# Optimization experiments

Measured on AMD Instinct MI355X. Metric: run time of the kernel, lower is better.

## Reference

```python
import jax, jax.numpy as jnp
import numpy as np

N, C, H, W = 1024, 16, 32, 32
E = 4096


def setup_inputs() -> dict:
    key = jax.random.key(0)
    ks = jax.random.split(key, 10)
    feats = jax.random.normal(ks[0], (N, C, H, W), dtype=jnp.float32)
    src = jax.random.randint(ks[1], (E,), 0, N)
    dst = jax.random.randint(ks[2], (E,), 0, N)
    sign = jax.random.randint(ks[3], (E,), 0, 2) * 2 - 1  # values in {-1, +1}
    edges = jnp.stack([src, sign, dst], axis=1).astype(jnp.int64)
    s = 0.05
    w1 = jax.random.normal(ks[4], (2 * C, 3 * C, 3, 3), dtype=jnp.float32) * s
    b1 = jnp.zeros((2 * C,), dtype=jnp.float32)
    w2 = jax.random.normal(ks[5], (2 * C, 2 * C, 3, 3), dtype=jnp.float32) * s
    b2 = jnp.zeros((2 * C,), dtype=jnp.float32)
    w3 = jax.random.normal(ks[6], (C, 2 * C, 3, 3), dtype=jnp.float32) * s
    b3 = jnp.zeros((C,), dtype=jnp.float32)
    return {"feats": feats, "edges": edges, "w1": w1, "b1": b1,
            "w2": w2, "b2": b2, "w3": w3, "b3": b3}


def _pool_edges(edges, feats, positive):
    # Bidirectional gather + scatter_add over selected edges.
    # Mask-by-zero keeps shapes static (equivalent math to torch.where selection).
    sign = edges[:, 1]
    mask = (sign > 0) if positive else (sign < 0)
    w = mask.astype(feats.dtype)[:, None, None, None]
    src = edges[:, 0]
    dst = edges[:, 2]
    pooled = jnp.zeros_like(feats)
    pooled = pooled.at[dst].add(feats[src] * w)  # src -> dst
    pooled = pooled.at[src].add(feats[dst] * w)  # dst -> src
    return pooled


def _conv(x, w, b):
    y = jax.lax.conv_general_dilated(
        x, w, window_strides=(1, 1), padding=((1, 1), (1, 1)),
        dimension_numbers=("NCHW", "OIHW", "NCHW"))
    return y + b[None, :, None, None]


def _leaky(x):
    return jax.nn.leaky_relu(x, negative_slope=0.1)


def reference(feats, edges, w1, b1, w2, b2, w3, b3):
    pos = _pool_edges(edges, feats, positive=True)
    neg = _pool_edges(edges, feats, positive=False)
    x = jnp.concatenate([feats, pos, neg], axis=1)  # [N, 3C, H, W]
    x = _leaky(_conv(x, w1, b1))
    x = _leaky(_conv(x, w2, b2))
    x = _leaky(_conv(x, w3, b3))
    return x
```

## Files before the change

kernel.cpp:

```cpp
#include <hip/hip_runtime.h>


#define NIMG 1024
#define CHW  16384
#define NEDGE 4096
#define MAXD 64

#define ICP1 56
#define KP1  456
#define ICP2 40
#define KP2  296
#define XSZ (34*34*ICP1)
#define WSZ (32*KP1)

#define WG1N (32*KP1)
#define WG2N (32*KP2)
#define WG3N (16*KP2)
#define WGTOT (WG1N+WG2N+WG3N)

typedef __attribute__((ext_vector_type(8))) _Float16 half8;
typedef __attribute__((ext_vector_type(4))) _Float16 half4;
typedef __attribute__((ext_vector_type(4))) float float4v;

__device__ __forceinline__ float leaky(float x) { return x > 0.f ? x : 0.1f * x; }

__global__ __launch_bounds__(256) void build_adj(
    const int* __restrict__ edges, int* __restrict__ deg, int* __restrict__ adj,
    const float* __restrict__ w1, const float* __restrict__ w2,
    const float* __restrict__ w3, _Float16* __restrict__ wg)
{
    const int e = blockIdx.x * 256 + threadIdx.x;
    const bool is64 = (edges[1] == 0);
    int s, sg, d;
    if (is64) { s = edges[6*e]; sg = edges[6*e + 2]; d = edges[6*e + 4]; }
    else      { s = edges[3*e]; sg = edges[3*e + 1]; d = edges[3*e + 2]; }
    const int tag_d = (d << 1) | (int)(sg > 0);
    const int tag_s = (s << 1) | (int)(sg > 0);
    int i = atomicAdd(&deg[s], 1); if (i < MAXD) adj[(s << 6) + i] = tag_d;
    int j = atomicAdd(&deg[d], 1); if (j < MAXD) adj[(d << 6) + j] = tag_s;

    for (int t = e; t < WGTOT; t += NEDGE) {
        _Float16 val = (_Float16)0.f;
        if (t < WG1N) {
            int oc = t / KP1, r = t - oc * KP1;
            if (r < 432) { int tap = r / 48, ic = r - tap * 48;
                           val = (_Float16)w1[(oc*48 + ic)*9 + tap]; }
        } else if (t < WG1N + WG2N) {
            int u = t - WG1N;
            int oc = u / KP2, r = u - oc * KP2;
            if (r < 288) { int tap = r / 32, ic = r - tap * 32;
                           val = (_Float16)w2[(oc*32 + ic)*9 + tap]; }
        } else {
            int u = t - (WG1N + WG2N);
            int oc = u / KP2, r = u - oc * KP2;
            if (r < 288) { int tap = r / 32, ic = r - tap * 32;
                           val = (_Float16)w3[(oc*32 + ic)*9 + tap]; }
        }
        wg[t] = val;
    }
}

__global__ __launch_bounds__(256) void transpose_kernel(
    const float* __restrict__ feats, _Float16* __restrict__ fcl)
{
    const int n = blockIdx.x, tid = threadIdx.x;
    const float* fb = feats + (size_t)n * CHW;
    _Float16*    ob = fcl   + (size_t)n * 1024 * 16;
    const int p0 = tid * 4;
    float4v t[16];
    #pragma unroll
    for (int c = 0; c < 16; ++c) t[c] = *(const float4v*)(fb + (c << 10) + p0);
    #pragma unroll
    for (int u = 0; u < 4; ++u) {
        half8 v0, v1;
        #pragma unroll
        for (int c = 0; c < 8; ++c) { v0[c] = (_Float16)t[c][u]; v1[c] = (_Float16)t[c+8][u]; }
        *(half8*)(ob + (p0+u)*16)     = v0;
        *(half8*)(ob + (p0+u)*16 + 8) = v1;
    }
}

__global__ __launch_bounds__(1024, 4) void conv_kernel(
    const _Float16* __restrict__ fcl,
    const int* __restrict__ deg, const int* __restrict__ adj,
    const _Float16* __restrict__ wg,
    const float* __restrict__ b1, const float* __restrict__ b2,
    const float* __restrict__ b3, float* __restrict__ out)
{
    __shared__ __align__(16) _Float16 Xs[XSZ];
    __shared__ __align__(16) _Float16 Ws[WSZ];
    const int n    = blockIdx.x;
    const int tid  = threadIdx.x;
    const int wave = tid >> 6;
    const int lane = tid & 63;
    const int col  = lane & 15;
    const int quad = lane >> 4;

    {
        const half8* fc = (const half8*)(fcl + (size_t)n * CHW);
        const int p = tid;
        const int base = (((p >> 5) + 1)*34 + (p & 31) + 1) * ICP1;
        *(half8*)(Xs + base)     = fc[2*p];
        *(half8*)(Xs + base + 8) = fc[2*p + 1];

        int m = deg[n]; if (m > MAXD) m = MAXD;
        const int* al = adj + (n << 6);
        float ap[16], an[16];
        #pragma unroll
        for (int c = 0; c < 16; ++c) { ap[c] = 0.f; an[c] = 0.f; }
        int i = 0;
        for (; i + 4 <= m; i += 4) {
            int v0 = al[i], v1 = al[i+1], v2 = al[i+2], v3 = al[i+3];
            const half8* f0 = (const half8*)(fcl + (size_t)(v0 >> 1) * CHW);
            const half8* f1 = (const half8*)(fcl + (size_t)(v1 >> 1) * CHW);
            const half8* f2 = (const half8*)(fcl + (size_t)(v2 >> 1) * CHW);
            const half8* f3 = (const half8*)(fcl + (size_t)(v3 >> 1) * CHW);
            half8 x00 = f0[2*p], x01 = f0[2*p+1];
            half8 x10 = f1[2*p], x11 = f1[2*p+1];
            half8 x20 = f2[2*p], x21 = f2[2*p+1];
            half8 x30 = f3[2*p], x31 = f3[2*p+1];
            if (v0 & 1) { for (int c = 0; c < 8; ++c) { ap[c] += (float)x00[c]; ap[c+8] += (float)x01[c]; } }
            else        { for (int c = 0; c < 8; ++c) { an[c] += (float)x00[c]; an[c+8] += (float)x01[c]; } }
            if (v1 & 1) { for (int c = 0; c < 8; ++c) { ap[c] += (float)x10[c]; ap[c+8] += (float)x11[c]; } }
            else        { for (int c = 0; c < 8; ++c) { an[c] += (float)x10[c]; an[c+8] += (float)x11[c]; } }
            if (v2 & 1) { for (int c = 0; c < 8; ++c) { ap[c] += (float)x20[c]; ap[c+8] += (float)x21[c]; } }
            else        { for (int c = 0; c < 8; ++c) { an[c] += (float)x20[c]; an[c+8] += (float)x21[c]; } }
            if (v3 & 1) { for (int c = 0; c < 8; ++c) { ap[c] += (float)x30[c]; ap[c+8] += (float)x31[c]; } }
            else        { for (int c = 0; c < 8; ++c) { an[c] += (float)x30[c]; an[c+8] += (float)x31[c]; } }
        }
        for (; i < m; ++i) {
            const int v = al[i];
            const half8* fb = (const half8*)(fcl + (size_t)(v >> 1) * CHW);
            half8 x0 = fb[2*p], x1 = fb[2*p + 1];
            if (v & 1) {
                #pragma unroll
                for (int c = 0; c < 8; ++c) { ap[c] += (float)x0[c]; ap[c+8] += (float)x1[c]; }
            } else {
                #pragma unroll
                for (int c = 0; c < 8; ++c) { an[c] += (float)x0[c]; an[c+8] += (float)x1[c]; }
            }
        }
        half8 h0, h1, h2, h3;
        #pragma unroll
        for (int c = 0; c < 8; ++c) { h0[c] = (_Float16)ap[c]; h1[c] = (_Float16)ap[c+8];
                                      h2[c] = (_Float16)an[c]; h3[c] = (_Float16)an[c+8]; }
        *(half8*)(Xs + base + 16) = h0;
        *(half8*)(Xs + base + 24) = h1;
        *(half8*)(Xs + base + 32) = h2;
        *(half8*)(Xs + base + 40) = h3;

        {
            const half8* src = (const half8*)wg;
            half8* dst = (half8*)Ws;
            for (int t = tid; t < WG1N/8; t += 1024) dst[t] = src[t];
        }
        if (tid < 132) {
            int hp, wp;
            if      (tid < 34)  { hp = 0;        wp = tid; }
            else if (tid < 68)  { hp = 33;       wp = tid - 34; }
            else if (tid < 100) { hp = tid - 67; wp = 0; }
            else                { hp = tid - 99; wp = 33; }
            int hb = (hp*34 + wp) * ICP1;
            #pragma unroll
            for (int t = 0; t < 6; ++t) *(half8*)(Xs + hb + t*8) = (half8)0;
        }
    }
    __syncthreads();

    float4v acc[2][4];

    {
        #pragma unroll
        for (int m = 0; m < 2; ++m)
            #pragma unroll
            for (int j = 0; j < 4; ++j) acc[m][j] = (float4v){0.f,0.f,0.f,0.f};
        int pixb[4];
        #pragma unroll
        for (int j = 0; j < 4; ++j) {
            int p = wave*64 + j*16 + col;
            pixb[j] = ((p >> 5)*34 + (p & 31)) * ICP1;
        }
        const int abase = col * KP1 + quad * 8;
        #pragma unroll
        for (int ks = 0; ks < 14; ++ks) {
            int kq  = ks*32 + quad*8;
            int tap = kq / 48;
            int off = 0;
            if (tap < 9) {
                int ic0 = kq - tap*48;
                int dh = tap / 3, dw = tap - dh*3;
                off = (dh*34 + dw)*ICP1 + ic0;
            }
            half8 a0 = *(const half8*)(Ws + abase + ks*32);
            half8 a1 = *(const half8*)(Ws + 16*KP1 + abase + ks*32);
            #pragma unroll
            for (int j = 0; j < 4; ++j) {
                half8 b = *(const half8*)(Xs + pixb[j] + off);
                acc[0][j] = __builtin_amdgcn_mfma_f32_16x16x32_f16(a0, b, acc[0][j], 0, 0, 0);
                acc[1][j] = __builtin_amdgcn_mfma_f32_16x16x32_f16(a1, b, acc[1][j], 0, 0, 0);
            }
        }
    }
    __syncthreads();

    {
        if (tid < 132) {
            int hp, wp;
            if      (tid < 34)  { hp = 0;        wp = tid; }
            else if (tid < 68)  { hp = 33;       wp = tid - 34; }
            else if (tid < 100) { hp = tid - 67; wp = 0; }
            else                { hp = tid - 99; wp = 33; }
            int hb = (hp*34 + wp) * ICP2;
            #pragma unroll
            for (int t = 0; t < 4; ++t) *(half8*)(Xs + hb + t*8) = (half8)0;
        }
        float bv[2][4];
        #pragma unroll
        for (int m = 0; m < 2; ++m)
            #pragma unroll
            for (int r = 0; r < 4; ++r) bv[m][r] = b1[m*16 + quad*4 + r];
        #pragma unroll
        for (int m = 0; m < 2; ++m)
            #pragma unroll
            for (int j = 0; j < 4; ++j) {
                int p = wave*64 + j*16 + col;
                _Float16* y = Xs + ((((p>>5)+1)*34) + (p&31) + 1)*ICP2 + m*16 + quad*4;
                half4 v;
                #pragma unroll
                for (int r = 0; r < 4; ++r) v[r] = (_Float16)leaky(acc[m][j][r] + bv[m][r]);
                *(half4*)y = v;
            }
        {
            const half8* src = (const half8*)(wg + WG1N);
            half8* dst = (half8*)Ws;
            for (int t = tid; t < WG2N/8; t += 1024) dst[t] = src[t];
        }
    }
    __syncthreads();

    {
        #pragma unroll
        for (int m = 0; m < 2; ++m)
            #pragma unroll
            for (int j = 0; j < 4; ++j) acc[m][j] = (float4v){0.f,0.f,0.f,0.f};
        int pixb[4];
        #pragma unroll
        for (int j = 0; j < 4; ++j) {
            int p = wave*64 + j*16 + col;
            pixb[j] = ((p >> 5)*34 + (p & 31)) * ICP2;
        }
        const int abase = col * KP2 + quad * 8;
        #pragma unroll
        for (int ks = 0; ks < 9; ++ks) {
            int kq  = ks*32 + quad*8;
            int tap = kq >> 5, ic0 = kq & 31;
            int dh = tap / 3, dw = tap - dh*3;
            int off = (dh*34 + dw)*ICP2 + ic0;
            half8 a0 = *(const half8*)(Ws + abase + ks*32);
            half8 a1 = *(const half8*)(Ws + 16*KP2 + abase + ks*32);
            #pragma unroll
            for (int j = 0; j < 4; ++j) {
                half8 b = *(const half8*)(Xs + pixb[j] + off);
                acc[0][j] = __builtin_amdgcn_mfma_f32_16x16x32_f16(a0, b, acc[0][j], 0, 0, 0);
                acc[1][j] = __builtin_amdgcn_mfma_f32_16x16x32_f16(a1, b, acc[1][j], 0, 0, 0);
            }
        }
    }
    __syncthreads();

    {
        float bv[2][4];
        #pragma unroll
        for (int m = 0; m < 2; ++m)
            #pragma unroll
            for (int r = 0; r < 4; ++r) bv[m][r] = b2[m*16 + quad*4 + r];
        #pragma unroll
        for (int m = 0; m < 2; ++m)
            #pragma unroll
            for (int j = 0; j < 4; ++j) {
                int p = wave*64 + j*16 + col;
                _Float16* y = Xs + ((((p>>5)+1)*34) + (p&31) + 1)*ICP2 + m*16 + quad*4;
                half4 v;
                #pragma unroll
                for (int r = 0; r < 4; ++r) v[r] = (_Float16)leaky(acc[m][j][r] + bv[m][r]);
                *(half4*)y = v;
            }
        {
            const half8* src = (const half8*)(wg + WG1N + WG2N);
            half8* dst = (half8*)Ws;
            for (int t = tid; t < WG3N/8; t += 1024) dst[t] = src[t];
        }
    }
    __syncthreads();

    {
        float4v a3[4];
        #pragma unroll
        for (int j = 0; j < 4; ++j) a3[j] = (float4v){0.f,0.f,0.f,0.f};
        int pixb[4];
        #pragma unroll
        for (int j = 0; j < 4; ++j) {
            int p = wave*64 + j*16 + col;
            pixb[j] = ((p >> 5)*34 + (p & 31)) * ICP2;
        }
        const int abase = col * KP2 + quad * 8;
        #pragma unroll
        for (int ks = 0; ks < 9; ++ks) {
            int kq  = ks*32 + quad*8;
            int tap = kq >> 5, ic0 = kq & 31;
            int dh = tap / 3, dw = tap - dh*3;
            int off = (dh*34 + dw)*ICP2 + ic0;
            half8 a0 = *(const half8*)(Ws + abase + ks*32);
            #pragma unroll
            for (int j = 0; j < 4; ++j) {
                half8 b = *(const half8*)(Xs + pixb[j] + off);
                a3[j] = __builtin_amdgcn_mfma_f32_16x16x32_f16(a0, b, a3[j], 0, 0, 0);
            }
        }
        float bv[4];
        #pragma unroll
        for (int r = 0; r < 4; ++r) bv[r] = b3[quad*4 + r];
        float* op = out + (size_t)n * CHW;
        #pragma unroll
        for (int j = 0; j < 4; ++j) {
            int p = wave*64 + j*16 + col;
            #pragma unroll
            for (int r = 0; r < 4; ++r)
                op[(quad*4 + r)*1024 + p] = leaky(a3[j][r] + bv[r]);
        }
    }
}

extern "C" void kernel_launch(void* const* d_in, const int* in_sizes, int n_in,
                              void* d_out, int out_size, void* d_ws, size_t ws_size,
                              hipStream_t stream) {
    const float* feats = (const float*)d_in[0];
    const int*   edges = (const int*)  d_in[1];
    const float* w1 = (const float*)d_in[2];
    const float* b1 = (const float*)d_in[3];
    const float* w2 = (const float*)d_in[4];
    const float* b2 = (const float*)d_in[5];
    const float* w3 = (const float*)d_in[6];
    const float* b3 = (const float*)d_in[7];
    float* out = (float*)d_out;

    _Float16* fcl = (_Float16*)d_ws;
    int* deg = (int*)((char*)d_ws + (32u << 20));
    int* adj = deg + NIMG;
    _Float16* wg = (_Float16*)((char*)d_ws + (32u << 20) + 4096 + NIMG*MAXD*4);

    hipMemsetAsync(deg, 0, NIMG * sizeof(int), stream);
    build_adj<<<dim3(NEDGE/256), dim3(256), 0, stream>>>(edges, deg, adj, w1, w2, w3, wg);
    transpose_kernel<<<dim3(NIMG), dim3(256), 0, stream>>>(feats, fcl);
    conv_kernel<<<dim3(NIMG), dim3(1024), 0, stream>>>(fcl, deg, adj, wg,
                                                       b1, b2, b3, out);
}
```

Before: 233.3 us.

## Halve conv block size, double pixels per wave, retile weights, merge prep kernels

The transpose and adjacency/weight-packing kernels are merged into one launch, removing a kernel launch. The conv kernel now uses 512 threads, with each wave covering 128 pixels (8 MFMA column tiles) so each A-fragment load is reused across twice as many MFMAs. Weights are repacked into a per-k-step [ks][oc][32] layout to replace the padded row-major layout. Each thread now gathers neighbor sums for two pixels, and register pressure roughly doubles for accumulators, which may reduce occupancy.

```diff
diff --git a/kernel.cpp b/kernel.cpp
--- a/kernel.cpp
+++ b/kernel.cpp
@@ -7,15 +7,13 @@
 #define MAXD 64
 
 #define ICP1 56
-#define KP1  456
 #define ICP2 40
-#define KP2  296
 #define XSZ (34*34*ICP1)
-#define WSZ (32*KP1)
-
-#define WG1N (32*KP1)
-#define WG2N (32*KP2)
-#define WG3N (16*KP2)
+#define WSZ (14*32*32)
+
+#define WG1N (14*32*32)
+#define WG2N (9*32*32)
+#define WG3N (9*16*32)
 #define WGTOT (WG1N+WG2N+WG3N)
 
 typedef __attribute__((ext_vector_type(8))) _Float16 half8;
@@ -24,12 +22,32 @@
 
 __device__ __forceinline__ float leaky(float x) { return x > 0.f ? x : 0.1f * x; }
 
-__global__ __launch_bounds__(256) void build_adj(
+__global__ __launch_bounds__(256) void prep_kernel(
+    const float* __restrict__ feats, _Float16* __restrict__ fcl,
     const int* __restrict__ edges, int* __restrict__ deg, int* __restrict__ adj,
     const float* __restrict__ w1, const float* __restrict__ w2,
     const float* __restrict__ w3, _Float16* __restrict__ wg)
 {
-    const int e = blockIdx.x * 256 + threadIdx.x;
+    const int b = blockIdx.x, tid = threadIdx.x;
+    if (b < NIMG) {
+        const int n = b;
+        const float* fb = feats + (size_t)n * CHW;
+        _Float16*    ob = fcl   + (size_t)n * 1024 * 16;
+        const int p0 = tid * 4;
+        float4v t[16];
+        #pragma unroll
+        for (int c = 0; c < 16; ++c) t[c] = *(const float4v*)(fb + (c << 10) + p0);
+        #pragma unroll
+        for (int u = 0; u < 4; ++u) {
+            half8 v0, v1;
+            #pragma unroll
+            for (int c = 0; c < 8; ++c) { v0[c] = (_Float16)t[c][u]; v1[c] = (_Float16)t[c+8][u]; }
+            *(half8*)(ob + (p0+u)*16)     = v0;
+            *(half8*)(ob + (p0+u)*16 + 8) = v1;
+        }
+        return;
+    }
+    const int e = (b - NIMG) * 256 + tid;
     const bool is64 = (edges[1] == 0);
     int s, sg, d;
     if (is64) { s = edges[6*e]; sg = edges[6*e + 2]; d = edges[6*e + 4]; }
@@ -42,45 +60,28 @@
     for (int t = e; t < WGTOT; t += NEDGE) {
         _Float16 val = (_Float16)0.f;
         if (t < WG1N) {
-            int oc = t / KP1, r = t - oc * KP1;
-            if (r < 432) { int tap = r / 48, ic = r - tap * 48;
+            int ks = t >> 10, oc = (t >> 5) & 31, j32 = t & 31;
+            int k = ks*32 + j32;
+            if (k < 432) { int tap = k / 48, ic = k - tap*48;
                            val = (_Float16)w1[(oc*48 + ic)*9 + tap]; }
         } else if (t < WG1N + WG2N) {
             int u = t - WG1N;
-            int oc = u / KP2, r = u - oc * KP2;
-            if (r < 288) { int tap = r / 32, ic = r - tap * 32;
-                           val = (_Float16)w2[(oc*32 + ic)*9 + tap]; }
+            int ks = u >> 10, oc = (u >> 5) & 31, j32 = u & 31;
+            int k = ks*32 + j32;
+            int tap = k >> 5, ic = k & 31;
+            val = (_Float16)w2[(oc*32 + ic)*9 + tap];
         } else {
             int u = t - (WG1N + WG2N);
-            int oc = u / KP2, r = u - oc * KP2;
-            if (r < 288) { int tap = r / 32, ic = r - tap * 32;
-                           val = (_Float16)w3[(oc*32 + ic)*9 + tap]; }
+            int ks = u >> 9, oc = (u >> 5) & 15, j32 = u & 31;
+            int k = ks*32 + j32;
+            int tap = k >> 5, ic = k & 31;
+            val = (_Float16)w3[(oc*32 + ic)*9 + tap];
         }
         wg[t] = val;
     }
 }
 
-__global__ __launch_bounds__(256) void transpose_kernel(
-    const float* __restrict__ feats, _Float16* __restrict__ fcl)
-{
-    const int n = blockIdx.x, tid = threadIdx.x;
-    const float* fb = feats + (size_t)n * CHW;
-    _Float16*    ob = fcl   + (size_t)n * 1024 * 16;
-    const int p0 = tid * 4;
-    float4v t[16];
-    #pragma unroll
-    for (int c = 0; c < 16; ++c) t[c] = *(const float4v*)(fb + (c << 10) + p0);
-    #pragma unroll
-    for (int u = 0; u < 4; ++u) {
-        half8 v0, v1;
-        #pragma unroll
-        for (int c = 0; c < 8; ++c) { v0[c] = (_Float16)t[c][u]; v1[c] = (_Float16)t[c+8][u]; }
-        *(half8*)(ob + (p0+u)*16)     = v0;
-        *(half8*)(ob + (p0+u)*16 + 8) = v1;
-    }
-}
-
-__global__ __launch_bounds__(1024, 4) void conv_kernel(
+__global__ __launch_bounds__(512, 2) void conv_kernel(
     const _Float16* __restrict__ fcl,
     const int* __restrict__ deg, const int* __restrict__ adj,
     const _Float16* __restrict__ wg,
@@ -98,61 +99,62 @@
 
     {
         const half8* fc = (const half8*)(fcl + (size_t)n * CHW);
-        const int p = tid;
-        const int base = (((p >> 5) + 1)*34 + (p & 31) + 1) * ICP1;
-        *(half8*)(Xs + base)     = fc[2*p];
-        *(half8*)(Xs + base + 8) = fc[2*p + 1];
-
         int m = deg[n]; if (m > MAXD) m = MAXD;
         const int* al = adj + (n << 6);
-        float ap[16], an[16];
-        #pragma unroll
-        for (int c = 0; c < 16; ++c) { ap[c] = 0.f; an[c] = 0.f; }
-        int i = 0;
-        for (; i + 4 <= m; i += 4) {
-            int v0 = al[i], v1 = al[i+1], v2 = al[i+2], v3 = al[i+3];
-            const half8* f0 = (const half8*)(fcl + (size_t)(v0 >> 1) * CHW);
-            const half8* f1 = (const half8*)(fcl + (size_t)(v1 >> 1) * CHW);
-            const half8* f2 = (const half8*)(fcl + (size_t)(v2 >> 1) * CHW);
-            const half8* f3 = (const half8*)(fcl + (size_t)(v3 >> 1) * CHW);
-            half8 x00 = f0[2*p], x01 = f0[2*p+1];
-            half8 x10 = f1[2*p], x11 = f1[2*p+1];
-            half8 x20 = f2[2*p], x21 = f2[2*p+1];
-            half8 x30 = f3[2*p], x31 = f3[2*p+1];
-            if (v0 & 1) { for (int c = 0; c < 8; ++c) { ap[c] += (float)x00[c]; ap[c+8] += (float)x01[c]; } }
-            else        { for (int c = 0; c < 8; ++c) { an[c] += (float)x00[c]; an[c+8] += (float)x01[c]; } }
-            if (v1 & 1) { for (int c = 0; c < 8; ++c) { ap[c] += (float)x10[c]; ap[c+8] += (float)x11[c]; } }
-            else        { for (int c = 0; c < 8; ++c) { an[c] += (float)x10[c]; an[c+8] += (float)x11[c]; } }
-            if (v2 & 1) { for (int c = 0; c < 8; ++c) { ap[c] += (float)x20[c]; ap[c+8] += (float)x21[c]; } }
-            else        { for (int c = 0; c < 8; ++c) { an[c] += (float)x20[c]; an[c+8] += (float)x21[c]; } }
-            if (v3 & 1) { for (int c = 0; c < 8; ++c) { ap[c] += (float)x30[c]; ap[c+8] += (float)x31[c]; } }
-            else        { for (int c = 0; c < 8; ++c) { an[c] += (float)x30[c]; an[c+8] += (float)x31[c]; } }
-        }
-        for (; i < m; ++i) {
-            const int v = al[i];
-            const half8* fb = (const half8*)(fcl + (size_t)(v >> 1) * CHW);
-            half8 x0 = fb[2*p], x1 = fb[2*p + 1];
-            if (v & 1) {
-                #pragma unroll
-                for (int c = 0; c < 8; ++c) { ap[c] += (float)x0[c]; ap[c+8] += (float)x1[c]; }
-            } else {
-                #pragma unroll
-                for (int c = 0; c < 8; ++c) { an[c] += (float)x0[c]; an[c+8] += (float)x1[c]; }
-            }
-        }
-        half8 h0, h1, h2, h3;
-        #pragma unroll
-        for (int c = 0; c < 8; ++c) { h0[c] = (_Float16)ap[c]; h1[c] = (_Float16)ap[c+8];
-                                      h2[c] = (_Float16)an[c]; h3[c] = (_Float16)an[c+8]; }
-        *(half8*)(Xs + base + 16) = h0;
-        *(half8*)(Xs + base + 24) = h1;
-        *(half8*)(Xs + base + 32) = h2;
-        *(half8*)(Xs + base + 40) = h3;
-
+        #pragma unroll 2
+        for (int h = 0; h < 2; ++h) {
+            const int p = tid + h*512;
+            const int base = (((p >> 5) + 1)*34 + (p & 31) + 1) * ICP1;
+            *(half8*)(Xs + base)     = fc[2*p];
+            *(half8*)(Xs + base + 8) = fc[2*p + 1];
+            float ap[16], an[16];
+            #pragma unroll
+            for (int c = 0; c < 16; ++c) { ap[c] = 0.f; an[c] = 0.f; }
+            int i = 0;
+            for (; i + 4 <= m; i += 4) {
+                int v0 = al[i], v1 = al[i+1], v2 = al[i+2], v3 = al[i+3];
+                const half8* f0 = (const half8*)(fcl + (size_t)(v0 >> 1) * CHW);
+                const half8* f1 = (const half8*)(fcl + (size_t)(v1 >> 1) * CHW);
+                const half8* f2 = (const half8*)(fcl + (size_t)(v2 >> 1) * CHW);
+                const half8* f3 = (const half8*)(fcl + (size_t)(v3 >> 1) * CHW);
+                half8 x00 = f0[2*p], x01 = f0[2*p+1];
+                half8 x10 = f1[2*p], x11 = f1[2*p+1];
+                half8 x20 = f2[2*p], x21 = f2[2*p+1];
+                half8 x30 = f3[2*p], x31 = f3[2*p+1];
+                if (v0 & 1) { for (int c = 0; c < 8; ++c) { ap[c] += (float)x00[c]; ap[c+8] += (float)x01[c]; } }
+                else        { for (int c = 0; c < 8; ++c) { an[c] += (float)x00[c]; an[c+8] += (float)x01[c]; } }
+                if (v1 & 1) { for (int c = 0; c < 8; ++c) { ap[c] += (float)x10[c]; ap[c+8] += (float)x11[c]; } }
+                else        { for (int c = 0; c < 8; ++c) { an[c] += (float)x10[c]; an[c+8] += (float)x11[c]; } }
+                if (v2 & 1) { for (int c = 0; c < 8; ++c) { ap[c] += (float)x20[c]; ap[c+8] += (float)x21[c]; } }
+                else        { for (int c = 0; c < 8; ++c) { an[c] += (float)x20[c]; an[c+8] += (float)x21[c]; } }
+                if (v3 & 1) { for (int c = 0; c < 8; ++c) { ap[c] += (float)x30[c]; ap[c+8] += (float)x31[c]; } }
+                else        { for (int c = 0; c < 8; ++c) { an[c] += (float)x30[c]; an[c+8] += (float)x31[c]; } }
+            }
+            for (; i < m; ++i) {
+                const int v = al[i];
+                const half8* fb = (const half8*)(fcl + (size_t)(v >> 1) * CHW);
+                half8 x0 = fb[2*p], x1 = fb[2*p + 1];
+                if (v & 1) {
+                    #pragma unroll
+                    for (int c = 0; c < 8; ++c) { ap[c] += (float)x0[c]; ap[c+8] += (float)x1[c]; }
+                } else {
+                    #pragma unroll
+                    for (int c = 0; c < 8; ++c) { an[c] += (float)x0[c]; an[c+8] += (float)x1[c]; }
+                }
+            }
+            half8 h0, h1, h2, h3;
+            #pragma unroll
+            for (int c = 0; c < 8; ++c) { h0[c] = (_Float16)ap[c]; h1[c] = (_Float16)ap[c+8];
+                                          h2[c] = (_Float16)an[c]; h3[c] = (_Float16)an[c+8]; }
+            *(half8*)(Xs + base + 16) = h0;
+            *(half8*)(Xs + base + 24) = h1;
+            *(half8*)(Xs + base + 32) = h2;
+            *(half8*)(Xs + base + 40) = h3;
+        }
         {
             const half8* src = (const half8*)wg;
             half8* dst = (half8*)Ws;
-            for (int t = tid; t < WG1N/8; t += 1024) dst[t] = src[t];
+            for (int t = tid; t < WG1N/8; t += 512) dst[t] = src[t];
         }
         if (tid < 132) {
             int hp, wp;
@@ -167,20 +169,20 @@
     }
     __syncthreads();
 
-    float4v acc[2][4];
-
-    {
-        #pragma unroll
-        for (int m = 0; m < 2; ++m)
-            #pragma unroll
-            for (int j = 0; j < 4; ++j) acc[m][j] = (float4v){0.f,0.f,0.f,0.f};
-        int pixb[4];
-        #pragma unroll
-        for (int j = 0; j < 4; ++j) {
-            int p = wave*64 + j*16 + col;
+    float4v acc[2][8];
+
+    {
+        #pragma unroll
+        for (int m = 0; m < 2; ++m)
+            #pragma unroll
+            for (int j = 0; j < 8; ++j) acc[m][j] = (float4v){0.f,0.f,0.f,0.f};
+        int pixb[8];
+        #pragma unroll
+        for (int j = 0; j < 8; ++j) {
+            int p = wave*128 + j*16 + col;
             pixb[j] = ((p >> 5)*34 + (p & 31)) * ICP1;
         }
-        const int abase = col * KP1 + quad * 8;
+        const int abase = col*32 + quad*8;
         #pragma unroll
         for (int ks = 0; ks < 14; ++ks) {
             int kq  = ks*32 + quad*8;
@@ -191,10 +193,10 @@
                 int dh = tap / 3, dw = tap - dh*3;
                 off = (dh*34 + dw)*ICP1 + ic0;
             }
-            half8 a0 = *(const half8*)(Ws + abase + ks*32);
-            half8 a1 = *(const half8*)(Ws + 16*KP1 + abase + ks*32);
-            #pragma unroll
-            for (int j = 0; j < 4; ++j) {
+            half8 a0 = *(const half8*)(Ws + ks*1024 + abase);
+            half8 a1 = *(const half8*)(Ws + ks*1024 + 512 + abase);
+            #pragma unroll
+            for (int j = 0; j < 8; ++j) {
                 half8 b = *(const half8*)(Xs + pixb[j] + off);
                 acc[0][j] = __builtin_amdgcn_mfma_f32_16x16x32_f16(a0, b, acc[0][j], 0, 0, 0);
                 acc[1][j] = __builtin_amdgcn_mfma_f32_16x16x32_f16(a1, b, acc[1][j], 0, 0, 0);
@@ -222,8 +224,8 @@
         #pragma unroll
         for (int m = 0; m < 2; ++m)
             #pragma unroll
-            for (int j = 0; j < 4; ++j) {
-                int p = wave*64 + j*16 + col;
+            for (int j = 0; j < 8; ++j) {
+                int p = wave*128 + j*16 + col;
                 _Float16* y = Xs + ((((p>>5)+1)*34) + (p&31) + 1)*ICP2 + m*16 + quad*4;
                 half4 v;
                 #pragma unroll
@@ -233,33 +235,33 @@
         {
             const half8* src = (const half8*)(wg + WG1N);
             half8* dst = (half8*)Ws;
-            for (int t = tid; t < WG2N/8; t += 1024) dst[t] = src[t];
-        }
-    }
-    __syncthreads();
-
-    {
-        #pragma unroll
-        for (int m = 0; m < 2; ++m)
-            #pragma unroll
-            for (int j = 0; j < 4; ++j) acc[m][j] = (float4v){0.f,0.f,0.f,0.f};
-        int pixb[4];
-        #pragma unroll
-        for (int j = 0; j < 4; ++j) {
-            int p = wave*64 + j*16 + col;
+            for (int t = tid; t < WG2N/8; t += 512) dst[t] = src[t];
+        }
+    }
+    __syncthreads();
+
+    {
+        #pragma unroll
+        for (int m = 0; m < 2; ++m)
+            #pragma unroll
+            for (int j = 0; j < 8; ++j) acc[m][j] = (float4v){0.f,0.f,0.f,0.f};
+        int pixb[8];
+        #pragma unroll
+        for (int j = 0; j < 8; ++j) {
+            int p = wave*128 + j*16 + col;
             pixb[j] = ((p >> 5)*34 + (p & 31)) * ICP2;
         }
-        const int abase = col * KP2 + quad * 8;
+        const int abase = col*32 + quad*8;
         #pragma unroll
         for (int ks = 0; ks < 9; ++ks) {
             int kq  = ks*32 + quad*8;
             int tap = kq >> 5, ic0 = kq & 31;
             int dh = tap / 3, dw = tap - dh*3;
             int off = (dh*34 + dw)*ICP2 + ic0;
-            half8 a0 = *(const half8*)(Ws + abase + ks*32);
-            half8 a1 = *(const half8*)(Ws + 16*KP2 + abase + ks*32);
-            #pragma unroll
-            for (int j = 0; j < 4; ++j) {
+            half8 a0 = *(const half8*)(Ws + ks*1024 + abase);
+            half8 a1 = *(const half8*)(Ws + ks*1024 + 512 + abase);
+            #pragma unroll
+            for (int j = 0; j < 8; ++j) {
                 half8 b = *(const half8*)(Xs + pixb[j] + off);
                 acc[0][j] = __builtin_amdgcn_mfma_f32_16x16x32_f16(a0, b, acc[0][j], 0, 0, 0);
                 acc[1][j] = __builtin_amdgcn_mfma_f32_16x16x32_f16(a1, b, acc[1][j], 0, 0, 0);
@@ -277,8 +279,8 @@
         #pragma unroll
         for (int m = 0; m < 2; ++m)
             #pragma unroll
-            for (int j = 0; j < 4; ++j) {
-                int p = wave*64 + j*16 + col;
+            for (int j = 0; j < 8; ++j) {
+                int p = wave*128 + j*16 + col;
                 _Float16* y = Xs + ((((p>>5)+1)*34) + (p&31) + 1)*ICP2 + m*16 + quad*4;
                 half4 v;
                 #pragma unroll
@@ -288,31 +290,31 @@
         {
             const half8* src = (const half8*)(wg + WG1N + WG2N);
             half8* dst = (half8*)Ws;
-            for (int t = tid; t < WG3N/8; t += 1024) dst[t] = src[t];
-        }
-    }
-    __syncthreads();
-
-    {
-        float4v a3[4];
-        #pragma unroll
-        for (int j = 0; j < 4; ++j) a3[j] = (float4v){0.f,0.f,0.f,0.f};
-        int pixb[4];
-        #pragma unroll
-        for (int j = 0; j < 4; ++j) {
-            int p = wave*64 + j*16 + col;
+            for (int t = tid; t < WG3N/8; t += 512) dst[t] = src[t];
+        }
+    }
+    __syncthreads();
+
+    {
+        float4v a3[8];
+        #pragma unroll
+        for (int j = 0; j < 8; ++j) a3[j] = (float4v){0.f,0.f,0.f,0.f};
+        int pixb[8];
+        #pragma unroll
+        for (int j = 0; j < 8; ++j) {
+            int p = wave*128 + j*16 + col;
             pixb[j] = ((p >> 5)*34 + (p & 31)) * ICP2;
         }
-        const int abase = col * KP2 + quad * 8;
+        const int abase = col*32 + quad*8;
         #pragma unroll
         for (int ks = 0; ks < 9; ++ks) {
             int kq  = ks*32 + quad*8;
             int tap = kq >> 5, ic0 = kq & 31;
             int dh = tap / 3, dw = tap - dh*3;
             int off = (dh*34 + dw)*ICP2 + ic0;
-            half8 a0 = *(const half8*)(Ws + abase + ks*32);
-            #pragma unroll
-            for (int j = 0; j < 4; ++j) {
+            half8 a0 = *(const half8*)(Ws + ks*512 + abase);
+            #pragma unroll
+            for (int j = 0; j < 8; ++j) {
                 half8 b = *(const half8*)(Xs + pixb[j] + off);
                 a3[j] = __builtin_amdgcn_mfma_f32_16x16x32_f16(a0, b, a3[j], 0, 0, 0);
             }
@@ -322,8 +324,8 @@
         for (int r = 0; r < 4; ++r) bv[r] = b3[quad*4 + r];
         float* op = out + (size_t)n * CHW;
         #pragma unroll
-        for (int j = 0; j < 4; ++j) {
-            int p = wave*64 + j*16 + col;
+        for (int j = 0; j < 8; ++j) {
+            int p = wave*128 + j*16 + col;
             #pragma unroll
             for (int r = 0; r < 4; ++r)
                 op[(quad*4 + r)*1024 + p] = leaky(a3[j][r] + bv[r]);
@@ -350,8 +352,8 @@
     _Float16* wg = (_Float16*)((char*)d_ws + (32u << 20) + 4096 + NIMG*MAXD*4);
 
     hipMemsetAsync(deg, 0, NIMG * sizeof(int), stream);
-    build_adj<<<dim3(NEDGE/256), dim3(256), 0, stream>>>(edges, deg, adj, w1, w2, w3, wg);
-    transpose_kernel<<<dim3(NIMG), dim3(256), 0, stream>>>(feats, fcl);
-    conv_kernel<<<dim3(NIMG), dim3(1024), 0, stream>>>(fcl, deg, adj, wg,
-                                                       b1, b2, b3, out);
+    prep_kernel<<<dim3(NIMG + NEDGE/256), dim3(256), 0, stream>>>(
+        feats, fcl, edges, deg, adj, w1, w2, w3, wg);
+    conv_kernel<<<dim3(NIMG), dim3(512), 0, stream>>>(fcl, deg, adj, wg,
+                                                      b1, b2, b3, out);
 }
```

Result: faster. 227.2 us (-2.6%).
